# Kernel tuning notes

Measured on AMD Instinct MI355X. Metric: run time of the kernel, lower is better.

Reference implementation:

```python
import jax, jax.numpy as jnp
import numpy as np

MARGIN = 0.2
NEG_SENTINEL = -1e30


def setup_inputs() -> dict:
    key = jax.random.key(0)
    k1, k2 = jax.random.split(key)
    batch_reprs = jax.random.normal(k1, (4096, 128), dtype=jnp.float32)
    batch_labels = jax.random.randint(k2, (4096,), 0, 512, dtype=jnp.int64 if jax.config.jax_enable_x64 else jnp.int32)
    return {"batch_reprs": batch_reprs, "batch_labels": batch_labels}


def _loss(batch_reprs, batch_labels):
    # class match matrix (self-similarity kept, as in original)
    match = (batch_labels[:, None] == batch_labels[None, :]).astype(batch_reprs.dtype)  # [B,B]

    # pairwise euclidean distance (squared=False), sim = -dist
    sq = jnp.sum(batch_reprs * batch_reprs, axis=1)
    d2 = jnp.maximum(sq[:, None] + sq[None, :] - 2.0 * (batch_reprs @ batch_reprs.T), 0.0)
    zero = (d2 == 0.0).astype(batch_reprs.dtype)
    dist = jnp.sqrt(d2 + zero * 1e-16) * (1.0 - zero)
    sim_hat = -dist + (1.0 - match) * MARGIN  # use_margin=True

    # rank positions via double argsort (descending)
    order = jnp.argsort(-sim_hat, axis=1)
    rank = jnp.argsort(order, axis=1).astype(sim_hat.dtype) + 1.0  # [B,B], 1-based ranks

    k = jnp.sum(match, axis=1, keepdims=True)                      # n_pos per row, [B,1]
    fp = (match < 1.0) & (rank <= k)                               # false positives
    fp_num = jnp.sum(fp, axis=1, keepdims=True).astype(sim_hat.dtype)
    fn = (match > 0.0) & (rank > k)                                # false negatives

    n = sim_hat.shape[1]
    # per-row top-(fp_num) false negatives by sim_hat, vectorized via masked sort
    fn_scores = jnp.where(fn, sim_hat, NEG_SENTINEL)
    idx = jnp.argsort(-fn_scores, axis=1)
    fn_sorted = jnp.take_along_axis(sim_hat, idx, axis=1)
    fn_ranks = jnp.take_along_axis(rank, idx, axis=1)
    fn_mask_sorted = jnp.take_along_axis(fn, idx, axis=1)
    sel = (jnp.arange(n)[None, :] < fp_num) & fn_mask_sorted       # top fp_num entries

    # weighted margins (rows with fp_num==0 contribute 0 automatically)
    fp_term = jnp.sum(jnp.where(fp, sim_hat * (0.5 + (k - rank + 1.0) / k * 0.5), 0.0))
    fn_term = jnp.sum(jnp.where(sel, fn_sorted * (0.5 + (fn_ranks - k) / (n - k) * 0.5), 0.0))
    return fp_term - fn_term


def reference(batch_reprs, batch_labels):
    return _loss(batch_reprs, batch_labels)
```

## Files before the change

### kernel.cpp

```cpp
#include <hip/hip_runtime.h>
#include <cstdint>
#include <cstddef>

#define B 4096
#define D 128
#define MARGIN_F 0.2f
#define CW 256

typedef short bf16x8 __attribute__((ext_vector_type(8)));
typedef float f32x4 __attribute__((ext_vector_type(4)));

__device__ __forceinline__ uint32_t xform_key(float f) {
    uint32_t u = __float_as_uint(f);
    return u ^ (uint32_t)((((int32_t)u) >> 31) | 0x80000000);
}
__device__ __forceinline__ float unxform16(uint32_t k16) {
    uint32_t u = k16 << 16;
    u = (u & 0x80000000u) ? (u ^ 0x80000000u) : ~u;
    return __uint_as_float(u);
}
__device__ __forceinline__ unsigned short f2bf(float f) {
    uint32_t u = __float_as_uint(f);
    return (unsigned short)((u + 0x7FFFu + ((u >> 16) & 1u)) >> 16);
}

__global__ __launch_bounds__(256) void sq_kernel(const float* __restrict__ R,
                                                 float* __restrict__ sq,
                                                 float* __restrict__ out) {
    if (blockIdx.x == 0 && threadIdx.x == 0) out[0] = 0.0f;
    int wave = threadIdx.x >> 6;
    int lane = threadIdx.x & 63;
    int row  = blockIdx.x * 4 + wave;
    const float2* R2 = (const float2*)R + (size_t)row * (D / 2);
    float2 v = R2[lane];
    float s = v.x * v.x + v.y * v.y;
#pragma unroll
    for (int off = 32; off > 0; off >>= 1) s += __shfl_down(s, off);
    if (lane == 0) sq[row] = s;
}

__global__ __launch_bounds__(256) void conv_kernel(const float* __restrict__ R,
                                                   unsigned short* __restrict__ Rb) {
    int idx = (blockIdx.x * 256 + threadIdx.x) * 4;
    float4 v = *(const float4*)(R + idx);
    ushort4 o;
    o.x = f2bf(v.x); o.y = f2bf(v.y); o.z = f2bf(v.z); o.w = f2bf(v.w);
    *(ushort4*)(Rb + idx) = o;
}

__global__ __launch_bounds__(256) void gemm_sim_v3(const unsigned short* __restrict__ Rb,
                                                   const float* __restrict__ sq,
                                                   const int* __restrict__ labels,
                                                   unsigned short* __restrict__ simk) {
    __shared__ unsigned short sEP[4][4608];

    const int tid  = threadIdx.x;
    const int wid  = tid >> 6, lane = tid & 63;
    const int q    = lane >> 4, t = lane & 15;
    const int Ay0  = blockIdx.y * 128;
    const int Bx0  = blockIdx.x * 128;
    const int m0   = (wid >> 1) * 64;
    const int n0   = (wid & 1) * 64;

    f32x4 acc[4][4];
#pragma unroll
    for (int mi = 0; mi < 4; ++mi)
#pragma unroll
        for (int ni = 0; ni < 4; ++ni) acc[mi][ni] = (f32x4)0.0f;

    const unsigned short* baseA = Rb + (size_t)(Ay0 + m0 + t) * D + q * 8;
    const unsigned short* baseB = Rb + (size_t)(Bx0 + n0 + t) * D + q * 8;

#pragma unroll
    for (int kq = 0; kq < 4; ++kq) {
        bf16x8 af[4], bfr[4];
#pragma unroll
        for (int mi = 0; mi < 4; ++mi)
            af[mi] = *(const bf16x8*)(baseA + (size_t)mi * 16 * D + kq * 32);
#pragma unroll
        for (int ni = 0; ni < 4; ++ni)
            bfr[ni] = *(const bf16x8*)(baseB + (size_t)ni * 16 * D + kq * 32);
#pragma unroll
        for (int mi = 0; mi < 4; ++mi)
#pragma unroll
            for (int ni = 0; ni < 4; ++ni)
                acc[mi][ni] = __builtin_amdgcn_mfma_f32_16x16x32_bf16(
                    af[mi], bfr[ni], acc[mi][ni], 0, 0, 0);
    }

    float sqc[4]; int lc[4];
#pragma unroll
    for (int ni = 0; ni < 4; ++ni) {
        sqc[ni] = sq[Bx0 + n0 + ni * 16 + t];
        lc[ni]  = labels[Bx0 + n0 + ni * 16 + t];
    }
#pragma unroll
    for (int mi = 0; mi < 4; ++mi) {
#pragma unroll
        for (int r = 0; r < 4; ++r) {
            int lrow = mi * 16 + q * 4 + r;
            int grow = Ay0 + m0 + lrow;
            float sqr = sq[grow];
            int   lr  = labels[grow];
#pragma unroll
            for (int ni = 0; ni < 4; ++ni) {
                float g  = acc[mi][ni][r];
                float d2 = fmaxf(sqr + sqc[ni] - 2.0f * g, 0.0f);
                float dist = (d2 > 0.0f) ? sqrtf(d2) : 0.0f;
                float s = -dist + ((lr == lc[ni]) ? 0.0f : MARGIN_F);
                uint32_t key = xform_key(s);
                sEP[wid][lrow * 72 + ni * 16 + t] =
                    (unsigned short)((key + 0x8000u) >> 16);
            }
        }
    }
#pragma unroll
    for (int it = 0; it < 8; ++it) {
        int rr = it * 8 + (lane >> 3);
        int cc = (lane & 7) * 8;
        uint4 v = *(uint4*)(&sEP[wid][rr * 72 + cc]);
        *(uint4*)(simk + (size_t)(Ay0 + m0 + rr) * B + Bx0 + n0 + cc) = v;
    }
}

__global__ __launch_bounds__(64, 4) void row_loss_w64(const unsigned short* __restrict__ simk,
                                                      const int* __restrict__ labels,
                                                      float* __restrict__ out) {
    __shared__ uint32_t cand_c[CW];
    __shared__ int cnt;

    const int lane = threadIdx.x;
    const int row  = blockIdx.x;
    if (lane == 0) cnt = 0;

    const uint4* pv = (const uint4*)(simk + (size_t)row * B);
    const int4*  lv = (const int4*)labels;
    const int li = labels[row];

    uint4 kv[8];
    uint64_t mbits = 0;
    uint32_t t1 = 0, t2 = 0;
#pragma unroll
    for (int q = 0; q < 8; ++q) {
        kv[q] = pv[q * 64 + lane];
        const int lb = (q * 64 + lane) * 2;
        int4 la = lv[lb], lc = lv[lb + 1];
        uint32_t u[8] = {kv[q].x & 0xFFFFu, kv[q].x >> 16,
                         kv[q].y & 0xFFFFu, kv[q].y >> 16,
                         kv[q].z & 0xFFFFu, kv[q].z >> 16,
                         kv[q].w & 0xFFFFu, kv[q].w >> 16};
#pragma unroll
        for (int c = 0; c < 8; ++c) {
            uint32_t mn = min(t1, u[c]);
            t1 = max(t1, u[c]);
            t2 = max(t2, mn);
        }
        mbits |= (uint64_t)(la.x == li) << (q * 8 + 0);
        mbits |= (uint64_t)(la.y == li) << (q * 8 + 1);
        mbits |= (uint64_t)(la.z == li) << (q * 8 + 2);
        mbits |= (uint64_t)(la.w == li) << (q * 8 + 3);
        mbits |= (uint64_t)(lc.x == li) << (q * 8 + 4);
        mbits |= (uint64_t)(lc.y == li) << (q * 8 + 5);
        mbits |= (uint64_t)(lc.z == li) << (q * 8 + 6);
        mbits |= (uint64_t)(lc.w == li) << (q * 8 + 7);
    }

    int kloc = __popcll(mbits);
#pragma unroll
    for (int off = 32; off > 0; off >>= 1) kloc += __shfl_xor(kloc, off);
    const int k = kloc;
    const float kf = (float)k;

    const int kneed = min(k, 128);
    uint32_t T = 0;
#pragma unroll
    for (int b = 15; b >= 0; --b) {
        uint32_t g = T | (1u << b);
        int c = __popcll(__ballot(t1 >= g)) + __popcll(__ballot(t2 >= g));
        if (c >= kneed) T = g;
    }
    const uint32_t combT = T << 12;

#pragma unroll
    for (int q = 0; q < 8; ++q) {
        uint32_t u[8] = {kv[q].x & 0xFFFFu, kv[q].x >> 16,
                         kv[q].y & 0xFFFFu, kv[q].y >> 16,
                         kv[q].z & 0xFFFFu, kv[q].z >> 16,
                         kv[q].w & 0xFFFFu, kv[q].w >> 16};
        int jb = (q * 64 + lane) * 8;
#pragma unroll
        for (int c = 0; c < 8; ++c) {
            int e = q * 8 + c;
            uint32_t m = (uint32_t)((mbits >> e) & 1);
            if (u[c] >= T || m) {
                int p = atomicAdd(&cnt, 1);
                if (p < CW)
                    cand_c[p] = (u[c] << 12) | (uint32_t)(4095 - (jb + c)) | (m << 31);
            }
        }
    }
    const int ncand = min(cnt, CW);

    float facc = 0.0f;

    for (int s = lane; s < ncand; s += 64) {
        uint32_t cs = cand_c[s];
        uint32_t comb = cs & 0x7FFFFFFFu;
        int m = (int)(cs >> 31);
        if (comb >= combT) {
            int c2 = 0;
            for (int c = 0; c < ncand; ++c)
                c2 += ((cand_c[c] & 0x7FFFFFFFu) > comb) ? 1 : 0;
            int rank = 1 + c2;
            float v = unxform16(comb >> 12);
            if (!m && rank <= k)
                facc += v * (0.5f + ((kf - (float)rank + 1.0f) / kf) * 0.5f);
            else if (m && rank > k)
                facc -= v * (0.5f + (((float)rank - kf) / (float)(B - k)) * 0.5f);
        }
    }

    uint32_t p0 = 0xFFFFFFFFu, p1 = 0xFFFFFFFFu, p2 = 0xFFFFFFFFu, p3 = 0xFFFFFFFFu;
    int np = 0;
    for (int c = 0; c <= ncand; ++c) {
        bool flushit = (c == ncand);
        if (!flushit) {
            uint32_t cc_ = cand_c[c];
            if ((cc_ & 0x80000000u) && (cc_ & 0x7FFFFFFFu) < combT) {
                uint32_t comb = cc_ & 0x7FFFFFFFu;
                if (np == 0) p0 = comb; else if (np == 1) p1 = comb;
                else if (np == 2) p2 = comb; else p3 = comb;
                ++np;
                flushit = (np == 4);
            }
        }
        if (flushit && np > 0) {
            int c0 = 0, c1 = 0, c2 = 0, c3 = 0;
#pragma unroll
            for (int q = 0; q < 8; ++q) {
                uint32_t u[8] = {kv[q].x & 0xFFFFu, kv[q].x >> 16,
                                 kv[q].y & 0xFFFFu, kv[q].y >> 16,
                                 kv[q].z & 0xFFFFu, kv[q].z >> 16,
                                 kv[q].w & 0xFFFFu, kv[q].w >> 16};
                int jb = (q * 64 + lane) * 8;
#pragma unroll
                for (int cc = 0; cc < 8; ++cc) {
                    uint32_t comb_e = (u[cc] << 12) | (uint32_t)(4095 - (jb + cc));
                    c0 += (comb_e > p0) ? 1 : 0;
                    c1 += (comb_e > p1) ? 1 : 0;
                    c2 += (comb_e > p2) ? 1 : 0;
                    c3 += (comb_e > p3) ? 1 : 0;
                }
            }
#pragma unroll
            for (int off = 32; off > 0; off >>= 1) {
                c0 += __shfl_xor(c0, off); c1 += __shfl_xor(c1, off);
                c2 += __shfl_xor(c2, off); c3 += __shfl_xor(c3, off);
            }
            if (lane == 0) {
                int rk[4] = {1 + c0, 1 + c1, 1 + c2, 1 + c3};
                uint32_t pp[4] = {p0, p1, p2, p3};
                for (int i = 0; i < np; ++i) {
                    float v = unxform16(pp[i] >> 12);
                    facc -= v * (0.5f + (((float)rk[i] - kf) / (float)(B - k)) * 0.5f);
                }
            }
            p0 = p1 = p2 = p3 = 0xFFFFFFFFu;
            np = 0;
        }
    }

#pragma unroll
    for (int off = 32; off > 0; off >>= 1) facc += __shfl_xor(facc, off);
    if (lane == 0) atomicAdd(out, facc);
}

extern "C" void kernel_launch(void* const* d_in, const int* in_sizes, int n_in,
                              void* d_out, int out_size, void* d_ws, size_t ws_size,
                              hipStream_t stream) {
    const float* R      = (const float*)d_in[0];
    const int*   labels = (const int*)d_in[1];
    float* out = (float*)d_out;

    float*          sq   = (float*)d_ws;
    unsigned short* Rb   = (unsigned short*)((char*)d_ws + 16 * 1024);
    unsigned short* simk = (unsigned short*)((char*)d_ws + 16 * 1024 + 1024 * 1024 + 256);

    hipLaunchKernelGGL(sq_kernel, dim3(B / 4), dim3(256), 0, stream, R, sq, out);
    hipLaunchKernelGGL(conv_kernel, dim3(B * D / 1024), dim3(256), 0, stream, R, Rb);
    hipLaunchKernelGGL(gemm_sim_v3, dim3(B / 128, B / 128), dim3(256), 0, stream,
                       Rb, sq, labels, simk);
    hipLaunchKernelGGL(row_loss_w64, dim3(B), dim3(64), 0, stream, simk, labels, out);
}
```

Before: 158.6 us.

## Fuse prep kernels, stage GEMM tiles in swizzled LDS, use nontemporal simk I/O

Merges the squared-norm and bf16 conversion kernels into one prep kernel, which saves a launch and a second read of R. The GEMM now stages the 128x128 A and B tiles into XOR-swizzled shared memory with cooperative loads, replacing strided global fragment loads. That shared buffer is reused for the epilogue. The simk matrix is written and read with nontemporal stores and loads to avoid polluting the cache, and the row-loss kernel raises its occupancy hint to 8 waves per SIMD and issues all row loads up front.

```diff
diff --git a/kernel.cpp b/kernel.cpp
--- a/kernel.cpp
+++ b/kernel.cpp
@@ -9,6 +9,7 @@
 
 typedef short bf16x8 __attribute__((ext_vector_type(8)));
 typedef float f32x4 __attribute__((ext_vector_type(4)));
+typedef uint32_t u32x4 __attribute__((ext_vector_type(4)));
 
 __device__ __forceinline__ uint32_t xform_key(float f) {
     uint32_t u = __float_as_uint(f);
@@ -24,35 +25,29 @@
     return (unsigned short)((u + 0x7FFFu + ((u >> 16) & 1u)) >> 16);
 }
 
-__global__ __launch_bounds__(256) void sq_kernel(const float* __restrict__ R,
-                                                 float* __restrict__ sq,
-                                                 float* __restrict__ out) {
+__global__ __launch_bounds__(256) void prep_kernel(const float* __restrict__ R,
+                                                   float* __restrict__ sq,
+                                                   unsigned short* __restrict__ Rb,
+                                                   float* __restrict__ out) {
     if (blockIdx.x == 0 && threadIdx.x == 0) out[0] = 0.0f;
     int wave = threadIdx.x >> 6;
     int lane = threadIdx.x & 63;
     int row  = blockIdx.x * 4 + wave;
     const float2* R2 = (const float2*)R + (size_t)row * (D / 2);
     float2 v = R2[lane];
+    ushort2 o; o.x = f2bf(v.x); o.y = f2bf(v.y);
+    *(ushort2*)(Rb + (size_t)row * D + lane * 2) = o;
     float s = v.x * v.x + v.y * v.y;
 #pragma unroll
     for (int off = 32; off > 0; off >>= 1) s += __shfl_down(s, off);
     if (lane == 0) sq[row] = s;
 }
 
-__global__ __launch_bounds__(256) void conv_kernel(const float* __restrict__ R,
-                                                   unsigned short* __restrict__ Rb) {
-    int idx = (blockIdx.x * 256 + threadIdx.x) * 4;
-    float4 v = *(const float4*)(R + idx);
-    ushort4 o;
-    o.x = f2bf(v.x); o.y = f2bf(v.y); o.z = f2bf(v.z); o.w = f2bf(v.w);
-    *(ushort4*)(Rb + idx) = o;
-}
-
-__global__ __launch_bounds__(256) void gemm_sim_v3(const unsigned short* __restrict__ Rb,
-                                                   const float* __restrict__ sq,
-                                                   const int* __restrict__ labels,
-                                                   unsigned short* __restrict__ simk) {
-    __shared__ unsigned short sEP[4][4608];
+__global__ __launch_bounds__(256) void gemm_sim_mfma(const unsigned short* __restrict__ Rb,
+                                                     const float* __restrict__ sq,
+                                                     const int* __restrict__ labels,
+                                                     unsigned short* __restrict__ simk) {
+    __shared__ unsigned short sAB[32768];
 
     const int tid  = threadIdx.x;
     const int wid  = tid >> 6, lane = tid & 63;
@@ -62,24 +57,38 @@
     const int m0   = (wid >> 1) * 64;
     const int n0   = (wid & 1) * 64;
 
+#pragma unroll
+    for (int it = 0; it < 16; ++it) {
+        int s = (wid * 16 + it) * 64 + lane;
+        int local = s & 2047;
+        int r = local >> 4;
+        int p = local & 15;
+        int srcrow = ((s < 2048) ? Ay0 : Bx0) + r;
+        const uint4* src = (const uint4*)(Rb + (size_t)srcrow * D + ((p ^ (r & 15)) << 3));
+        *(uint4*)(&sAB[(size_t)s * 8]) = *src;
+    }
+    __syncthreads();
+
     f32x4 acc[4][4];
 #pragma unroll
     for (int mi = 0; mi < 4; ++mi)
 #pragma unroll
         for (int ni = 0; ni < 4; ++ni) acc[mi][ni] = (f32x4)0.0f;
-
-    const unsigned short* baseA = Rb + (size_t)(Ay0 + m0 + t) * D + q * 8;
-    const unsigned short* baseB = Rb + (size_t)(Bx0 + n0 + t) * D + q * 8;
 
 #pragma unroll
     for (int kq = 0; kq < 4; ++kq) {
         bf16x8 af[4], bfr[4];
-#pragma unroll
-        for (int mi = 0; mi < 4; ++mi)
-            af[mi] = *(const bf16x8*)(baseA + (size_t)mi * 16 * D + kq * 32);
-#pragma unroll
-        for (int ni = 0; ni < 4; ++ni)
-            bfr[ni] = *(const bf16x8*)(baseB + (size_t)ni * 16 * D + kq * 32);
+        const int ksw = (kq * 4 + q);
+#pragma unroll
+        for (int mi = 0; mi < 4; ++mi) {
+            int r = m0 + mi * 16 + t;
+            af[mi] = *(bf16x8*)(&sAB[(size_t)r * 128 + ((ksw ^ t) << 3)]);
+        }
+#pragma unroll
+        for (int ni = 0; ni < 4; ++ni) {
+            int r = n0 + ni * 16 + t;
+            bfr[ni] = *(bf16x8*)(&sAB[16384 + (size_t)r * 128 + ((ksw ^ t) << 3)]);
+        }
 #pragma unroll
         for (int mi = 0; mi < 4; ++mi)
 #pragma unroll
@@ -88,6 +97,9 @@
                     af[mi], bfr[ni], acc[mi][ni], 0, 0, 0);
     }
 
+    __syncthreads();
+
+    const int epi0 = wid * 4608;
     float sqc[4]; int lc[4];
 #pragma unroll
     for (int ni = 0; ni < 4; ++ni) {
@@ -109,7 +121,7 @@
                 float dist = (d2 > 0.0f) ? sqrtf(d2) : 0.0f;
                 float s = -dist + ((lr == lc[ni]) ? 0.0f : MARGIN_F);
                 uint32_t key = xform_key(s);
-                sEP[wid][lrow * 72 + ni * 16 + t] =
+                sAB[epi0 + lrow * 72 + ni * 16 + t] =
                     (unsigned short)((key + 0x8000u) >> 16);
             }
         }
@@ -118,12 +130,13 @@
     for (int it = 0; it < 8; ++it) {
         int rr = it * 8 + (lane >> 3);
         int cc = (lane & 7) * 8;
-        uint4 v = *(uint4*)(&sEP[wid][rr * 72 + cc]);
-        *(uint4*)(simk + (size_t)(Ay0 + m0 + rr) * B + Bx0 + n0 + cc) = v;
-    }
-}
-
-__global__ __launch_bounds__(64, 4) void row_loss_w64(const unsigned short* __restrict__ simk,
+        u32x4 v = *(u32x4*)(&sAB[epi0 + rr * 72 + cc]);
+        __builtin_nontemporal_store(
+            v, (u32x4*)(simk + (size_t)(Ay0 + m0 + rr) * B + Bx0 + n0 + cc));
+    }
+}
+
+__global__ __launch_bounds__(64, 8) void row_loss_w64(const unsigned short* __restrict__ simk,
                                                       const int* __restrict__ labels,
                                                       float* __restrict__ out) {
     __shared__ uint32_t cand_c[CW];
@@ -133,16 +146,19 @@
     const int row  = blockIdx.x;
     if (lane == 0) cnt = 0;
 
-    const uint4* pv = (const uint4*)(simk + (size_t)row * B);
+    const u32x4* pv = (const u32x4*)(simk + (size_t)row * B);
     const int4*  lv = (const int4*)labels;
     const int li = labels[row];
 
-    uint4 kv[8];
+    u32x4 kv[8];
+#pragma unroll
+    for (int q = 0; q < 8; ++q)
+        kv[q] = __builtin_nontemporal_load(pv + q * 64 + lane);
+
     uint64_t mbits = 0;
     uint32_t t1 = 0, t2 = 0;
 #pragma unroll
     for (int q = 0; q < 8; ++q) {
-        kv[q] = pv[q * 64 + lane];
         const int lb = (q * 64 + lane) * 2;
         int4 la = lv[lb], lc = lv[lb + 1];
         uint32_t u[8] = {kv[q].x & 0xFFFFu, kv[q].x >> 16,
@@ -286,9 +302,8 @@
     unsigned short* Rb   = (unsigned short*)((char*)d_ws + 16 * 1024);
     unsigned short* simk = (unsigned short*)((char*)d_ws + 16 * 1024 + 1024 * 1024 + 256);
 
-    hipLaunchKernelGGL(sq_kernel, dim3(B / 4), dim3(256), 0, stream, R, sq, out);
-    hipLaunchKernelGGL(conv_kernel, dim3(B * D / 1024), dim3(256), 0, stream, R, Rb);
-    hipLaunchKernelGGL(gemm_sim_v3, dim3(B / 128, B / 128), dim3(256), 0, stream,
+    hipLaunchKernelGGL(prep_kernel, dim3(B / 4), dim3(256), 0, stream, R, sq, Rb, out);
+    hipLaunchKernelGGL(gemm_sim_mfma, dim3(B / 128, B / 128), dim3(256), 0, stream,
                        Rb, sq, labels, simk);
     hipLaunchKernelGGL(row_loss_w64, dim3(B), dim3(64), 0, stream, simk, labels, out);
 }
```

Measured after the change: 192.1 us. 1.21x slower.
